# Optimization experiments

Measured on AMD Instinct MI355X. Metric: run time of the kernel, lower is better.

## Reference

```python
import jax, jax.numpy as jnp
import numpy as np

N_TOP = 5  # self.n from __init__
EPS = 1e-10


def setup_inputs() -> dict:
    key = jax.random.key(0)
    k1, k2 = jax.random.split(key)
    support_set = jax.random.normal(k1, (8, 4096, 64), dtype=jnp.float32)
    query_set = jax.random.normal(k2, (8, 4096, 64), dtype=jnp.float32)
    return {"support_set": support_set, "query_set": query_set, "bshot": 2048}


def reference(support_set, query_set, bshot):
    # support_set: [B,S,D], query_set: [B,Q,D]
    sum_support = jnp.sum(support_set * support_set, axis=2)          # [B,S]
    support_magnitude = jax.lax.rsqrt(jnp.clip(sum_support, EPS))     # clamp(eps, inf).rsqrt()
    dot = jnp.einsum('bqd,bsd->bqs', query_set, support_set)          # [B,Q,S]
    cos = dot * support_magnitude[:, None, :]                         # scale per support column
    top_vals, _ = jax.lax.top_k(cos[:, :, :bshot], N_TOP)             # [B,Q,n]
    return jnp.concatenate([top_vals, cos[:, :, bshot:]], axis=2)     # [B,Q,n+(S-bshot)]
```

## Files before the change

kernel.cpp:

```cpp
#include <hip/hip_runtime.h>
#include <hip/hip_bf16.h>

#define B_ 8
#define S_ 4096
#define Q_ 4096
#define D_ 64

typedef __attribute__((ext_vector_type(8))) short short8;
typedef __attribute__((ext_vector_type(4))) float f32x4;

__device__ __forceinline__ unsigned short f2bf(float f) {
  union { float f; unsigned u; } v; v.f = f;
  unsigned u = v.u;
  u += 0x7FFFu + ((u >> 16) & 1u);
  return (unsigned short)(u >> 16);
}

__global__ void prep_kernel(const float* __restrict__ supp,
                            const float* __restrict__ query,
                            unsigned short* __restrict__ supp_bf,
                            unsigned short* __restrict__ query_bf) {
  int r = blockIdx.x * blockDim.x + threadIdx.x;
  const int nsupp = B_ * S_;
  const int total = nsupp + B_ * Q_;
  if (r >= total) return;
  const bool is_supp = r < nsupp;
  const float* src = is_supp ? (supp + (size_t)r * D_)
                             : (query + (size_t)(r - nsupp) * D_);
  unsigned short* dst = is_supp ? (supp_bf + (size_t)r * D_)
                                : (query_bf + (size_t)(r - nsupp) * D_);
  float4 v[D_ / 4];
  float sum = 0.f;
#pragma unroll
  for (int i = 0; i < D_ / 4; ++i) {
    v[i] = ((const float4*)src)[i];
    sum += v[i].x * v[i].x + v[i].y * v[i].y + v[i].z * v[i].z + v[i].w * v[i].w;
  }
  const float sc = is_supp ? rsqrtf(fmaxf(sum, 1e-10f)) : 1.0f;
#pragma unroll
  for (int i = 0; i < D_ / 4; ++i) {
    ushort4 h;
    h.x = f2bf(v[i].x * sc); h.y = f2bf(v[i].y * sc);
    h.z = f2bf(v[i].z * sc); h.w = f2bf(v[i].w * sc);
    ((ushort4*)dst)[i] = h;
  }
}

__device__ __forceinline__ void ins5(float (&t)[5], float v) {
  float a = v, b;
  b = fminf(t[0], a); t[0] = fmaxf(t[0], a); a = b;
  b = fminf(t[1], a); t[1] = fmaxf(t[1], a); a = b;
  b = fminf(t[2], a); t[2] = fmaxf(t[2], a); a = b;
  b = fminf(t[3], a); t[3] = fmaxf(t[3], a); a = b;
  t[4] = fmaxf(t[4], a);
}

__global__ void cos_topk_kernel(const unsigned short* __restrict__ supp_bf,
                                const unsigned short* __restrict__ query_bf,
                                const int* __restrict__ pbshot,
                                float* __restrict__ out) {
  const int bs = *pbshot;
  const int OW = 5 + S_ - bs;

  const int b  = blockIdx.x >> 6;
  const int q0 = (blockIdx.x & 63) * 64;
  const int tid  = threadIdx.x;
  const int w    = tid >> 6;
  const int lane = tid & 63;
  const int l15  = lane & 15;
  const int l4   = lane >> 4;

  const int nt_top = bs >> 6;
  const int role = blockIdx.y;
  const bool is_top = (role == 0);
  int t0, t1;
  if (is_top) { t0 = 0; t1 = nt_top; }
  else {
    const int ct = (S_ >> 6) - nt_top;
    t0 = nt_top + (ct * (role - 1)) / 6;
    t1 = nt_top + (ct * role) / 6;
  }

  __shared__ unsigned short lds[2][64 * 64];

  const int qrow = q0 + w * 16 + l15;
  const unsigned short* qbase = query_bf + (size_t)(b * Q_ + qrow) * D_;
  const short8 a0 = *(const short8*)(qbase + l4 * 8);
  const short8 a1 = *(const short8*)(qbase + 32 + l4 * 8);

  float tk[4][5];
#pragma unroll
  for (int r2 = 0; r2 < 4; ++r2)
#pragma unroll
    for (int j = 0; j < 5; ++j) tk[r2][j] = -INFINITY;

  const int srow  = tid >> 2;
  const int chunk = tid & 3;
  const unsigned short* gstage0 =
      supp_bf + ((size_t)b * S_ + srow) * D_ + chunk * 16;
  const int dsw0 = srow * 64 + ((chunk * 16 + 0) ^ ((srow & 7) << 3));
  const int dsw1 = srow * 64 + ((chunk * 16 + 8) ^ ((srow & 7) << 3));

  uint4 st0 = *(const uint4*)(gstage0 + (size_t)t0 * 64 * D_);
  uint4 st1 = *(const uint4*)(gstage0 + (size_t)t0 * 64 * D_ + 8);
  *(uint4*)&lds[0][dsw0] = st0;
  *(uint4*)&lds[0][dsw1] = st1;

  const int rbase = b * Q_ + q0 + w * 16 + l4 * 4;
  float* obase = out + (size_t)rbase * OW + 5 - bs + l15;

  for (int t = t0; t < t1; ++t) {
    const int buf = (t - t0) & 1;
    if (t + 1 < t1) {
      const unsigned short* g = gstage0 + (size_t)(t + 1) * 64 * D_;
      st0 = *(const uint4*)(g);
      st1 = *(const uint4*)(g + 8);
    }
    __syncthreads();

    f32x4 ab[4];
#pragma unroll
    for (int fc = 0; fc < 4; ++fc) {
      const int scol = fc * 16 + l15;
      const int idx0 = scol * 64 + ((l4 * 8) ^ ((scol & 7) << 3));
      const int idx1 = scol * 64 + ((32 + l4 * 8) ^ ((scol & 7) << 3));
      const short8 b0 = *(const short8*)&lds[buf][idx0];
      const short8 b1 = *(const short8*)&lds[buf][idx1];
      f32x4 acc = {0.f, 0.f, 0.f, 0.f};
      acc = __builtin_amdgcn_mfma_f32_16x16x32_bf16(a0, b0, acc, 0, 0, 0);
      acc = __builtin_amdgcn_mfma_f32_16x16x32_bf16(a1, b1, acc, 0, 0, 0);

      if (is_top) {
#pragma unroll
        for (int r2 = 0; r2 < 4; ++r2) ins5(tk[r2], acc[r2]);
      } else {
        ab[fc] = acc;
      }
    }

    if (!is_top) {
#pragma unroll
      for (int r2 = 0; r2 < 4; ++r2) {
        float* rowp = obase + (size_t)r2 * OW + t * 64;
#pragma unroll
        for (int fc = 0; fc < 4; ++fc) rowp[fc * 16] = ab[fc][r2];
      }
    }

    if (t + 1 < t1) {
      *(uint4*)&lds[buf ^ 1][dsw0] = st0;
      *(uint4*)&lds[buf ^ 1][dsw1] = st1;
    }
  }

  if (is_top) {
#pragma unroll
    for (int m = 1; m <= 8; m <<= 1) {
#pragma unroll
      for (int r2 = 0; r2 < 4; ++r2) {
        float o0 = __shfl_xor(tk[r2][0], m);
        float o1 = __shfl_xor(tk[r2][1], m);
        float o2 = __shfl_xor(tk[r2][2], m);
        float o3 = __shfl_xor(tk[r2][3], m);
        float o4 = __shfl_xor(tk[r2][4], m);
        ins5(tk[r2], o0); ins5(tk[r2], o1); ins5(tk[r2], o2);
        ins5(tk[r2], o3); ins5(tk[r2], o4);
      }
    }
    if (l15 == 0) {
#pragma unroll
      for (int r2 = 0; r2 < 4; ++r2) {
        float* op = out + (size_t)(rbase + r2) * OW;
        op[0] = tk[r2][0]; op[1] = tk[r2][1]; op[2] = tk[r2][2];
        op[3] = tk[r2][3]; op[4] = tk[r2][4];
      }
    }
  }
}

extern "C" void kernel_launch(void* const* d_in, const int* in_sizes, int n_in,
                              void* d_out, int out_size, void* d_ws, size_t ws_size,
                              hipStream_t stream) {
  const float* supp  = (const float*)d_in[0];
  const float* query = (const float*)d_in[1];
  const int* pbshot  = (const int*)d_in[2];
  float* out = (float*)d_out;

  unsigned short* supp_bf  = (unsigned short*)d_ws;
  unsigned short* query_bf = supp_bf + (size_t)B_ * S_ * D_;

  const int rows = B_ * (S_ + Q_);
  prep_kernel<<<(rows + 255) / 256, 256, 0, stream>>>(supp, query, supp_bf,
                                                      query_bf);
  dim3 grid(B_ * (Q_ / 64), 7);
  cos_topk_kernel<<<grid, 256, 0, stream>>>(supp_bf, query_bf, pbshot, out);
}
```

Baseline: 87.09 us.

## Pre-pack support into MFMA fragment layout and read directly from global

The prep kernel now writes normalized bf16 support rows in a layout that matches the MFMA B-fragment lane order, so the main kernel loads B operands straight from global/L2 with coalesced 16-byte loads. The LDS double-buffer, its staging stores and the per-tile __syncthreads are removed. Block indices are also remapped so that consecutive blocks cycle through batches, which changes how work is spread across XCDs and caches. The trade-off is that each wave reloads the support tiles from cache without sharing them through LDS, so performance depends on L2 bandwidth and hit rate, and the prep kernel's stores become more scattered.

```diff
diff --git a/kernel.cpp b/kernel.cpp
--- a/kernel.cpp
+++ b/kernel.cpp
@@ -18,7 +18,7 @@
 
 __global__ void prep_kernel(const float* __restrict__ supp,
                             const float* __restrict__ query,
-                            unsigned short* __restrict__ supp_bf,
+                            unsigned short* __restrict__ packed,
                             unsigned short* __restrict__ query_bf) {
   int r = blockIdx.x * blockDim.x + threadIdx.x;
   const int nsupp = B_ * S_;
@@ -27,22 +27,34 @@
   const bool is_supp = r < nsupp;
   const float* src = is_supp ? (supp + (size_t)r * D_)
                              : (query + (size_t)(r - nsupp) * D_);
-  unsigned short* dst = is_supp ? (supp_bf + (size_t)r * D_)
-                                : (query_bf + (size_t)(r - nsupp) * D_);
-  float4 v[D_ / 4];
+  float4 v[16];
   float sum = 0.f;
 #pragma unroll
-  for (int i = 0; i < D_ / 4; ++i) {
+  for (int i = 0; i < 16; ++i) {
     v[i] = ((const float4*)src)[i];
     sum += v[i].x * v[i].x + v[i].y * v[i].y + v[i].z * v[i].z + v[i].w * v[i].w;
   }
   const float sc = is_supp ? rsqrtf(fmaxf(sum, 1e-10f)) : 1.0f;
+  unsigned us[32];
 #pragma unroll
-  for (int i = 0; i < D_ / 4; ++i) {
-    ushort4 h;
-    h.x = f2bf(v[i].x * sc); h.y = f2bf(v[i].y * sc);
-    h.z = f2bf(v[i].z * sc); h.w = f2bf(v[i].w * sc);
-    ((ushort4*)dst)[i] = h;
+  for (int i = 0; i < 16; ++i) {
+    us[2 * i]     = (unsigned)f2bf(v[i].x * sc) | ((unsigned)f2bf(v[i].y * sc) << 16);
+    us[2 * i + 1] = (unsigned)f2bf(v[i].z * sc) | ((unsigned)f2bf(v[i].w * sc) << 16);
+  }
+  if (is_supp) {
+    const int b = r >> 12, rb = r & (S_ - 1);
+    const int s16 = rb >> 4, l15 = rb & 15;
+    unsigned* pb = (unsigned*)(packed + ((size_t)(b * 256 + s16)) * 1024);
+#pragma unroll
+    for (int g = 0; g < 8; ++g) {
+      unsigned* dst = pb + ((g & 4) ? 256 : 0) + (l15 + (g & 3) * 16) * 4;
+      uint4 wd = {us[4 * g], us[4 * g + 1], us[4 * g + 2], us[4 * g + 3]};
+      *(uint4*)dst = wd;
+    }
+  } else {
+    unsigned* dst = (unsigned*)(query_bf + (size_t)(r - nsupp) * D_);
+#pragma unroll
+    for (int i = 0; i < 32; ++i) dst[i] = us[i];
   }
 }
 
@@ -55,15 +67,16 @@
   t[4] = fmaxf(t[4], a);
 }
 
-__global__ void cos_topk_kernel(const unsigned short* __restrict__ supp_bf,
+__global__ void cos_topk_kernel(const unsigned short* __restrict__ packed,
                                 const unsigned short* __restrict__ query_bf,
                                 const int* __restrict__ pbshot,
                                 float* __restrict__ out) {
   const int bs = *pbshot;
   const int OW = 5 + S_ - bs;
 
-  const int b  = blockIdx.x >> 6;
-  const int q0 = (blockIdx.x & 63) * 64;
+  const int bx = (blockIdx.x & 7) * 64 + (blockIdx.x >> 3);
+  const int b  = bx >> 6;
+  const int q0 = (bx & 63) * 64;
   const int tid  = threadIdx.x;
   const int w    = tid >> 6;
   const int lane = tid & 63;
@@ -81,8 +94,6 @@
     t1 = nt_top + (ct * role) / 6;
   }
 
-  __shared__ unsigned short lds[2][64 * 64];
-
   const int qrow = q0 + w * 16 + l15;
   const unsigned short* qbase = query_bf + (size_t)(b * Q_ + qrow) * D_;
   const short8 a0 = *(const short8*)(qbase + l4 * 8);
@@ -94,38 +105,19 @@
 #pragma unroll
     for (int j = 0; j < 5; ++j) tk[r2][j] = -INFINITY;
 
-  const int srow  = tid >> 2;
-  const int chunk = tid & 3;
-  const unsigned short* gstage0 =
-      supp_bf + ((size_t)b * S_ + srow) * D_ + chunk * 16;
-  const int dsw0 = srow * 64 + ((chunk * 16 + 0) ^ ((srow & 7) << 3));
-  const int dsw1 = srow * 64 + ((chunk * 16 + 8) ^ ((srow & 7) << 3));
-
-  uint4 st0 = *(const uint4*)(gstage0 + (size_t)t0 * 64 * D_);
-  uint4 st1 = *(const uint4*)(gstage0 + (size_t)t0 * 64 * D_ + 8);
-  *(uint4*)&lds[0][dsw0] = st0;
-  *(uint4*)&lds[0][dsw1] = st1;
+  const unsigned short* pbase = packed + (size_t)b * 256 * 1024 + lane * 8;
 
   const int rbase = b * Q_ + q0 + w * 16 + l4 * 4;
   float* obase = out + (size_t)rbase * OW + 5 - bs + l15;
 
   for (int t = t0; t < t1; ++t) {
-    const int buf = (t - t0) & 1;
-    if (t + 1 < t1) {
-      const unsigned short* g = gstage0 + (size_t)(t + 1) * 64 * D_;
-      st0 = *(const uint4*)(g);
-      st1 = *(const uint4*)(g + 8);
-    }
-    __syncthreads();
-
     f32x4 ab[4];
 #pragma unroll
     for (int fc = 0; fc < 4; ++fc) {
-      const int scol = fc * 16 + l15;
-      const int idx0 = scol * 64 + ((l4 * 8) ^ ((scol & 7) << 3));
-      const int idx1 = scol * 64 + ((32 + l4 * 8) ^ ((scol & 7) << 3));
-      const short8 b0 = *(const short8*)&lds[buf][idx0];
-      const short8 b1 = *(const short8*)&lds[buf][idx1];
+      const int sub = t * 4 + fc;
+      const unsigned short* p = pbase + (size_t)sub * 1024;
+      const short8 b0 = *(const short8*)(p);
+      const short8 b1 = *(const short8*)(p + 512);
       f32x4 acc = {0.f, 0.f, 0.f, 0.f};
       acc = __builtin_amdgcn_mfma_f32_16x16x32_bf16(a0, b0, acc, 0, 0, 0);
       acc = __builtin_amdgcn_mfma_f32_16x16x32_bf16(a1, b1, acc, 0, 0, 0);
@@ -145,11 +137,6 @@
 #pragma unroll
         for (int fc = 0; fc < 4; ++fc) rowp[fc * 16] = ab[fc][r2];
       }
-    }
-
-    if (t + 1 < t1) {
-      *(uint4*)&lds[buf ^ 1][dsw0] = st0;
-      *(uint4*)&lds[buf ^ 1][dsw1] = st1;
     }
   }
 
@@ -186,12 +173,12 @@
   const int* pbshot  = (const int*)d_in[2];
   float* out = (float*)d_out;
 
-  unsigned short* supp_bf  = (unsigned short*)d_ws;
-  unsigned short* query_bf = supp_bf + (size_t)B_ * S_ * D_;
+  unsigned short* packed   = (unsigned short*)d_ws;
+  unsigned short* query_bf = packed + (size_t)B_ * S_ * D_;
 
   const int rows = B_ * (S_ + Q_);
-  prep_kernel<<<(rows + 255) / 256, 256, 0, stream>>>(supp, query, supp_bf,
+  prep_kernel<<<(rows + 255) / 256, 256, 0, stream>>>(supp, query, packed,
                                                       query_bf);
   dim3 grid(B_ * (Q_ / 64), 7);
-  cos_topk_kernel<<<grid, 256, 0, stream>>>(supp_bf, query_bf, pbshot, out);
+  cos_topk_kernel<<<grid, 256, 0, stream>>>(packed, query_bf, pbshot, out);
 }
```

New measurement: 104.8 us. 1.2x slower.
